# Performance work log

Hardware: AMD Instinct MI355X
Metric: run time of the kernel (lower is better)

Reference implementation:

```python
import jax, jax.numpy as jnp
import numpy as np

EPS = 1e-5


def _segment_norm(x, seg, num_segments):
    # x: [N, D], seg: [N] sorted segment ids in [0, num_segments)
    ones = jnp.ones((x.shape[0],), x.dtype)
    cnt = jax.ops.segment_sum(ones, seg, num_segments=num_segments)      # [B]
    safe = jnp.maximum(cnt, 1.0)[:, None]                                # avoid 0-div
    mean = jax.ops.segment_sum(x, seg, num_segments=num_segments) / safe # [B, D]
    centered = x - mean[seg]
    var = jax.ops.segment_sum(centered * centered, seg, num_segments=num_segments) / safe
    std = jnp.sqrt(var)                                                  # unbiased=False
    normed = centered / (std[seg] + EPS)
    # graphs with a single element are passed through unchanged
    return jnp.where((cnt > 1.0)[seg][:, None], normed, x)


def setup_inputs() -> dict:
    key = jax.random.key(0)
    k1, k2, k3, k4 = jax.random.split(key, 4)
    N, D, B = 1_000_000, 128, 1024
    node_feat = jax.random.normal(k1, (N, D), dtype=jnp.float32)
    edge_feat = jax.random.normal(k2, (N, D), dtype=jnp.float32)
    node_seg = jnp.sort(jax.random.randint(k3, (N,), 0, B, dtype=jnp.int32))
    edge_seg = jnp.sort(jax.random.randint(k4, (N,), 0, B, dtype=jnp.int32))
    return {
        "node_feat": node_feat,
        "edge_feat": edge_feat,
        "node_gamma": jnp.ones((D,), jnp.float32),
        "node_beta": jnp.zeros((D,), jnp.float32),
        "edge_gamma": jnp.ones((D,), jnp.float32),
        "edge_beta": jnp.zeros((D,), jnp.float32),
        "node_seg": node_seg,
        "edge_seg": edge_seg,
        "num_graphs": B,
    }


def reference(node_feat, edge_feat, node_gamma, node_beta, edge_gamma, edge_beta,
              node_seg, edge_seg, num_graphs):
    node_out = _segment_norm(node_feat, node_seg, num_graphs) * node_gamma + node_beta
    edge_out = _segment_norm(edge_feat, edge_seg, num_graphs) * edge_gamma + edge_beta
    return (node_out, edge_out)
```

## Files before the change

### kernel.cpp

```cpp
#include <hip/hip_runtime.h>


static constexpr int   D4     = 32;
static constexpr int   CHUNK  = 64;
static constexpr int   NCHUNK = 4;
static constexpr int   TILE_W = CHUNK * NCHUNK;
static constexpr int   TILE_B = TILE_W * 4;
static constexpr int   DEPTH  = 4;
static constexpr float EPS    = 1e-5f;

typedef float vfloat4 __attribute__((ext_vector_type(4)));

#define WAITV(N) do { asm volatile("s_waitcnt vmcnt(" #N ")" ::: "memory"); \
                      __builtin_amdgcn_sched_barrier(0); } while (0)

__device__ __forceinline__ void waitv_dyn(int n) {
    switch (n) {
        case 0:  WAITV(0);  break;
        case 4:  WAITV(4);  break;
        case 8:  WAITV(8);  break;
        case 12: WAITV(12); break;
        case 16: WAITV(16); break;
        case 20: WAITV(20); break;
        default: WAITV(24); break;
    }
}

__device__ __forceinline__ void nt_store4(float4* p, const float4& v) {
    vfloat4 w = { v.x, v.y, v.z, v.w };
    __builtin_nontemporal_store(w, reinterpret_cast<vfloat4*>(p));
}

__device__ __forceinline__ void acc4(float4& s, float4& q, const float4& v) {
    s.x += v.x; s.y += v.y; s.z += v.z; s.w += v.w;
    q.x += v.x * v.x; q.y += v.y * v.y;
    q.z += v.z * v.z; q.w += v.w * v.w;
}

__device__ __forceinline__ float4 affine4(const float4& v, const float4& A,
                                          const float4& Bc) {
    float4 o;
    o.x = v.x * A.x + Bc.x; o.y = v.y * A.y + Bc.y;
    o.z = v.z * A.z + Bc.z; o.w = v.w * A.w + Bc.w;
    return o;
}

__global__ __launch_bounds__(256) void seg_norm_deep(
    const float4* __restrict__ xn, const float4* __restrict__ xe,
    const float*  __restrict__ gn, const float*  __restrict__ bn,
    const float*  __restrict__ ge, const float*  __restrict__ be,
    const int*    __restrict__ sn, const int*    __restrict__ se,
    float4* __restrict__ on, float4* __restrict__ oe,
    int N)
{
    __shared__ float4 stage[4][DEPTH][TILE_W];
    __shared__ float4 redS[256], redQ[256];
    __shared__ int    s_bounds[2];

    const bool is_edge = (blockIdx.y != 0);
    const float4* __restrict__ x   = is_edge ? xe : xn;
    const float*  __restrict__ gam = is_edge ? ge : gn;
    const float*  __restrict__ bet = is_edge ? be : bn;
    const int*    __restrict__ seg = is_edge ? se : sn;
    float4*       __restrict__ out = is_edge ? oe : on;

    const int b   = (int)blockIdx.x;
    const int tid = (int)threadIdx.x;

    if (tid < 2) {
        const int target = b + tid;
        int lo = 0, hi = N;
        while (lo < hi) {
            int mid = (lo + hi) >> 1;
            if (seg[mid] < target) lo = mid + 1; else hi = mid;
        }
        s_bounds[tid] = lo;
    }
    __syncthreads();
    const int start = s_bounds[0];
    const int end   = s_bounds[1];
    const int cnt   = end - start;
    if (cnt <= 0) return;

    const int w    = tid >> 6;
    const int lane = tid & 63;
    const int dg   = tid & 31;

    const size_t f4base = (size_t)start * D4;
    const int    f4cnt  = cnt * D4;
    const int    nt     = f4cnt / TILE_B;

    auto issue = [&](int t, float4* lp) {
        const float4* gp = x + f4base + (size_t)t * TILE_B + w * TILE_W + lane;
        #pragma unroll
        for (int i = 0; i < NCHUNK; ++i)
            __builtin_amdgcn_global_load_lds(gp + i * CHUNK, lp + i * CHUNK, 16, 0, 0);
    };

    float4 s = make_float4(0.f, 0.f, 0.f, 0.f);
    float4 q = make_float4(0.f, 0.f, 0.f, 0.f);
    if (nt > 0) {
        const int pre = min(nt, DEPTH);
        for (int p = 0; p < pre; ++p) issue(p, &stage[w][p][0]);
        for (int t = 0; t < nt; ++t) {
            waitv_dyn(4 * min(3, nt - 1 - t));
            float4* cur = &stage[w][t & (DEPTH - 1)][0];
            #pragma unroll
            for (int i = 0; i < NCHUNK; ++i)
                acc4(s, q, cur[i * CHUNK + lane]);
            if (t + DEPTH < nt) issue(t + DEPTH, cur);
        }
    }
    for (int j = nt * TILE_B + tid; j < f4cnt; j += 256)
        acc4(s, q, x[f4base + j]);

    redS[tid] = s; redQ[tid] = q;
    __syncthreads();

    if (tid < 32) {
        float4 S = redS[tid], Q = redQ[tid];
        #pragma unroll
        for (int k = 1; k < 8; ++k) {
            const float4 a = redS[k * 32 + tid], c = redQ[k * 32 + tid];
            S.x += a.x; S.y += a.y; S.z += a.z; S.w += a.w;
            Q.x += c.x; Q.y += c.y; Q.z += c.z; Q.w += c.w;
        }
        const float rc = 1.0f / (float)cnt;
        float4 m, iv;
        m.x = S.x * rc; m.y = S.y * rc; m.z = S.z * rc; m.w = S.w * rc;
        iv.x = 1.0f / (sqrtf(fmaxf(Q.x * rc - m.x * m.x, 0.f)) + EPS);
        iv.y = 1.0f / (sqrtf(fmaxf(Q.y * rc - m.y * m.y, 0.f)) + EPS);
        iv.z = 1.0f / (sqrtf(fmaxf(Q.z * rc - m.z * m.z, 0.f)) + EPS);
        iv.w = 1.0f / (sqrtf(fmaxf(Q.w * rc - m.w * m.w, 0.f)) + EPS);
        if (cnt <= 1) {
            m = make_float4(0.f, 0.f, 0.f, 0.f);
            iv = make_float4(1.f, 1.f, 1.f, 1.f);
        }
        const float4 g4 = ((const float4*)gam)[tid];
        const float4 b4 = ((const float4*)bet)[tid];
        float4 A, Bc;
        A.x = iv.x * g4.x; A.y = iv.y * g4.y; A.z = iv.z * g4.z; A.w = iv.w * g4.w;
        Bc.x = b4.x - m.x * A.x; Bc.y = b4.y - m.y * A.y;
        Bc.z = b4.z - m.z * A.z; Bc.w = b4.w - m.w * A.w;
        redS[tid] = A; redQ[tid] = Bc;
    }
    __syncthreads();
    const float4 A  = redS[dg];
    const float4 Bc = redQ[dg];
    __syncthreads();

    if (nt > 0) {
        const int pre = min(nt, DEPTH);
        for (int p = 0; p < pre; ++p) issue(p, &stage[w][p][0]);
        for (int t = 0; t < nt; ++t) {
            waitv_dyn(4 * min(3, nt - 1 - t) + 4 * min(3, t));
            float4* cur = &stage[w][t & (DEPTH - 1)][0];
            float4* op  = out + f4base + (size_t)t * TILE_B + w * TILE_W + lane;
            #pragma unroll
            for (int i = 0; i < NCHUNK; ++i)
                nt_store4(op + i * CHUNK, affine4(cur[i * CHUNK + lane], A, Bc));
            if (t + DEPTH < nt) issue(t + DEPTH, cur);
        }
    }
    for (int j = nt * TILE_B + tid; j < f4cnt; j += 256)
        nt_store4(&out[f4base + j], affine4(x[f4base + j], A, Bc));
}

extern "C" void kernel_launch(void* const* d_in, const int* in_sizes, int n_in,
                              void* d_out, int out_size, void* d_ws, size_t ws_size,
                              hipStream_t stream) {
    const float* node_feat  = (const float*)d_in[0];
    const float* edge_feat  = (const float*)d_in[1];
    const float* node_gamma = (const float*)d_in[2];
    const float* node_beta  = (const float*)d_in[3];
    const float* edge_gamma = (const float*)d_in[4];
    const float* edge_beta  = (const float*)d_in[5];
    const int*   node_seg   = (const int*)d_in[6];
    const int*   edge_seg   = (const int*)d_in[7];

    const int D = in_sizes[2];
    const int N = in_sizes[0] / D;
    const int B = 1024;

    float* out_node = (float*)d_out;
    float* out_edge = out_node + (size_t)N * (size_t)D;

    dim3 grid((unsigned)B, 2);
    seg_norm_deep<<<grid, 256, 0, stream>>>(
        (const float4*)node_feat, (const float4*)edge_feat,
        node_gamma, node_beta, edge_gamma, edge_beta,
        node_seg, edge_seg,
        (float4*)out_node, (float4*)out_edge, N);
}
```

Baseline: 488.8 us.

## Process four segments per block, overlapping next stats pass with previous write pass

Each block now handles two node segments and two edge segments in sequence, 512 blocks instead of 2048. The statistics pass of the next segment runs in the same loop as the normalize-and-store pass of the previous one, both streaming through LDS, so reads and writes overlap within a block. This targets idle bandwidth between each segment's two phases. In exchange, grid parallelism drops to 512 blocks, per-segment pipeline depth falls from 4 to 2, and the loop has more control logic.

```diff
diff --git a/kernel.cpp b/kernel.cpp
--- a/kernel.cpp
+++ b/kernel.cpp
@@ -6,7 +6,6 @@
 static constexpr int   NCHUNK = 4;
 static constexpr int   TILE_W = CHUNK * NCHUNK;
 static constexpr int   TILE_B = TILE_W * 4;
-static constexpr int   DEPTH  = 4;
 static constexpr float EPS    = 1e-5f;
 
 typedef float vfloat4 __attribute__((ext_vector_type(4)));
@@ -45,7 +44,7 @@
     return o;
 }
 
-__global__ __launch_bounds__(256) void seg_norm_deep(
+__global__ __launch_bounds__(256) void seg_norm_k4(
     const float4* __restrict__ xn, const float4* __restrict__ xe,
     const float*  __restrict__ gn, const float*  __restrict__ bn,
     const float*  __restrict__ ge, const float*  __restrict__ be,
@@ -53,117 +52,161 @@
     float4* __restrict__ on, float4* __restrict__ oe,
     int N)
 {
-    __shared__ float4 stage[4][DEPTH][TILE_W];
+    __shared__ float4 stage[4][4][TILE_W];
     __shared__ float4 redS[256], redQ[256];
-    __shared__ int    s_bounds[2];
-
-    const bool is_edge = (blockIdx.y != 0);
-    const float4* __restrict__ x   = is_edge ? xe : xn;
-    const float*  __restrict__ gam = is_edge ? ge : gn;
-    const float*  __restrict__ bet = is_edge ? be : bn;
-    const int*    __restrict__ seg = is_edge ? se : sn;
-    float4*       __restrict__ out = is_edge ? oe : on;
-
-    const int b   = (int)blockIdx.x;
-    const int tid = (int)threadIdx.x;
-
-    if (tid < 2) {
-        const int target = b + tid;
+    __shared__ int    sb[8];
+
+    const int k    = (int)blockIdx.x;
+    const int tid  = (int)threadIdx.x;
+    const int w    = tid >> 6;
+    const int lane = tid & 63;
+    const int dg   = tid & 31;
+
+    if (tid < 8) {
+        const int t      = tid >> 1;
+        const int* sg    = (t < 2) ? sn : se;
+        const int target = 2 * k + (t & 1) + (tid & 1);
         int lo = 0, hi = N;
         while (lo < hi) {
             int mid = (lo + hi) >> 1;
-            if (seg[mid] < target) lo = mid + 1; else hi = mid;
-        }
-        s_bounds[tid] = lo;
+            if (sg[mid] < target) lo = mid + 1; else hi = mid;
+        }
+        sb[tid] = lo;
     }
     __syncthreads();
-    const int start = s_bounds[0];
-    const int end   = s_bounds[1];
-    const int cnt   = end - start;
-    if (cnt <= 0) return;
-
-    const int w    = tid >> 6;
-    const int lane = tid & 63;
-    const int dg   = tid & 31;
-
-    const size_t f4base = (size_t)start * D4;
-    const int    f4cnt  = cnt * D4;
-    const int    nt     = f4cnt / TILE_B;
-
-    auto issue = [&](int t, float4* lp) {
-        const float4* gp = x + f4base + (size_t)t * TILE_B + w * TILE_W + lane;
+
+    auto issue = [&](const float4* src, size_t fb, int t, float4* lp) {
+        const float4* gp = src + fb + (size_t)t * TILE_B + w * TILE_W + lane;
         #pragma unroll
         for (int i = 0; i < NCHUNK; ++i)
             __builtin_amdgcn_global_load_lds(gp + i * CHUNK, lp + i * CHUNK, 16, 0, 0);
     };
 
-    float4 s = make_float4(0.f, 0.f, 0.f, 0.f);
-    float4 q = make_float4(0.f, 0.f, 0.f, 0.f);
-    if (nt > 0) {
-        const int pre = min(nt, DEPTH);
-        for (int p = 0; p < pre; ++p) issue(p, &stage[w][p][0]);
-        for (int t = 0; t < nt; ++t) {
-            waitv_dyn(4 * min(3, nt - 1 - t));
-            float4* cur = &stage[w][t & (DEPTH - 1)][0];
-            #pragma unroll
-            for (int i = 0; i < NCHUNK; ++i)
-                acc4(s, q, cur[i * CHUNK + lane]);
-            if (t + DEPTH < nt) issue(t + DEPTH, cur);
+    const float4* wx = nullptr;  float4* wo = nullptr;
+    size_t wfb = 0;  int wfc = 0, wnt = 0;
+    float4 Aw = make_float4(0,0,0,0), Bw = make_float4(0,0,0,0);
+
+    for (int ph = 0; ph <= 4; ++ph) {
+        const bool hasS = (ph < 4), hasW = (ph > 0);
+
+        const float4* sx = nullptr;
+        size_t sfb = 0;  int sfc = 0, snt = 0, scnt = 0;
+        if (hasS) {
+            sx = (ph < 2) ? xn : xe;
+            const int st = sb[2 * ph], en = sb[2 * ph + 1];
+            scnt = en - st;
+            sfb  = (size_t)st * D4;
+            sfc  = scnt * D4;
+            snt  = sfc / TILE_B;
+        }
+
+        float4 s = make_float4(0,0,0,0), q = make_float4(0,0,0,0);
+
+        if (hasS && hasW) {
+            const int tmid = min(snt, wnt);
+            if (tmid > 0) {
+                issue(sx, sfb, 0, &stage[w][0][0]);
+                issue(wx, wfb, 0, &stage[w][2][0]);
+                if (tmid > 1) {
+                    issue(sx, sfb, 1, &stage[w][1][0]);
+                    issue(wx, wfb, 1, &stage[w][3][0]);
+                }
+                for (int t = 0; t < tmid; ++t) {
+                    waitv_dyn(8 * min(1, tmid - 1 - t) + 4 * min(1, t));
+                    float4* sc = &stage[w][t & 1][0];
+                    float4* wc = &stage[w][2 + (t & 1)][0];
+                    float4* op = wo + wfb + (size_t)t * TILE_B + w * TILE_W + lane;
+                    #pragma unroll
+                    for (int i = 0; i < NCHUNK; ++i) {
+                        acc4(s, q, sc[i * CHUNK + lane]);
+                        nt_store4(op + i * CHUNK,
+                                  affine4(wc[i * CHUNK + lane], Aw, Bw));
+                    }
+                    if (t + 2 < tmid) {
+                        issue(sx, sfb, t + 2, sc);
+                        issue(wx, wfb, t + 2, wc);
+                    }
+                }
+                WAITV(0);
+            }
+            for (int j = tmid * TILE_B + tid; j < sfc; j += 256)
+                acc4(s, q, sx[sfb + j]);
+            for (int j = tmid * TILE_B + tid; j < wfc; j += 256)
+                nt_store4(&wo[wfb + j], affine4(wx[wfb + j], Aw, Bw));
+        } else if (hasS) {
+            if (snt > 0) {
+                const int pre = min(snt, 4);
+                for (int p = 0; p < pre; ++p) issue(sx, sfb, p, &stage[w][p][0]);
+                for (int t = 0; t < snt; ++t) {
+                    waitv_dyn(4 * min(3, snt - 1 - t));
+                    float4* cur = &stage[w][t & 3][0];
+                    #pragma unroll
+                    for (int i = 0; i < NCHUNK; ++i)
+                        acc4(s, q, cur[i * CHUNK + lane]);
+                    if (t + 4 < snt) issue(sx, sfb, t + 4, cur);
+                }
+            }
+            for (int j = snt * TILE_B + tid; j < sfc; j += 256)
+                acc4(s, q, sx[sfb + j]);
+        } else {
+            if (wnt > 0) {
+                const int pre = min(wnt, 4);
+                for (int p = 0; p < pre; ++p) issue(wx, wfb, p, &stage[w][p][0]);
+                for (int t = 0; t < wnt; ++t) {
+                    waitv_dyn(4 * min(3, wnt - 1 - t) + 4 * min(3, t));
+                    float4* cur = &stage[w][t & 3][0];
+                    float4* op  = wo + wfb + (size_t)t * TILE_B + w * TILE_W + lane;
+                    #pragma unroll
+                    for (int i = 0; i < NCHUNK; ++i)
+                        nt_store4(op + i * CHUNK,
+                                  affine4(cur[i * CHUNK + lane], Aw, Bw));
+                    if (t + 4 < wnt) issue(wx, wfb, t + 4, cur);
+                }
+            }
+            for (int j = wnt * TILE_B + tid; j < wfc; j += 256)
+                nt_store4(&wo[wfb + j], affine4(wx[wfb + j], Aw, Bw));
+        }
+
+        if (hasS) {
+            __syncthreads();
+            redS[tid] = s; redQ[tid] = q;
+            __syncthreads();
+            if (tid < 32) {
+                float4 S = redS[tid], Q = redQ[tid];
+                #pragma unroll
+                for (int j = 1; j < 8; ++j) {
+                    const float4 a = redS[j * 32 + tid], c = redQ[j * 32 + tid];
+                    S.x += a.x; S.y += a.y; S.z += a.z; S.w += a.w;
+                    Q.x += c.x; Q.y += c.y; Q.z += c.z; Q.w += c.w;
+                }
+                const float rc = 1.0f / (float)max(scnt, 1);
+                float4 m, iv;
+                m.x = S.x * rc; m.y = S.y * rc; m.z = S.z * rc; m.w = S.w * rc;
+                iv.x = 1.0f / (sqrtf(fmaxf(Q.x * rc - m.x * m.x, 0.f)) + EPS);
+                iv.y = 1.0f / (sqrtf(fmaxf(Q.y * rc - m.y * m.y, 0.f)) + EPS);
+                iv.z = 1.0f / (sqrtf(fmaxf(Q.z * rc - m.z * m.z, 0.f)) + EPS);
+                iv.w = 1.0f / (sqrtf(fmaxf(Q.w * rc - m.w * m.w, 0.f)) + EPS);
+                if (scnt <= 1) {
+                    m  = make_float4(0.f, 0.f, 0.f, 0.f);
+                    iv = make_float4(1.f, 1.f, 1.f, 1.f);
+                }
+                const float* gm = (ph < 2) ? gn : ge;
+                const float* bt = (ph < 2) ? bn : be;
+                const float4 g4 = ((const float4*)gm)[tid];
+                const float4 b4 = ((const float4*)bt)[tid];
+                float4 A, Bc;
+                A.x = iv.x * g4.x; A.y = iv.y * g4.y;
+                A.z = iv.z * g4.z; A.w = iv.w * g4.w;
+                Bc.x = b4.x - m.x * A.x; Bc.y = b4.y - m.y * A.y;
+                Bc.z = b4.z - m.z * A.z; Bc.w = b4.w - m.w * A.w;
+                redS[tid] = A; redQ[tid] = Bc;
+            }
+            __syncthreads();
+            Aw = redS[dg]; Bw = redQ[dg];
+            wx = sx; wo = (ph < 2) ? on : oe;
+            wfb = sfb; wfc = sfc; wnt = snt;
         }
     }
-    for (int j = nt * TILE_B + tid; j < f4cnt; j += 256)
-        acc4(s, q, x[f4base + j]);
-
-    redS[tid] = s; redQ[tid] = q;
-    __syncthreads();
-
-    if (tid < 32) {
-        float4 S = redS[tid], Q = redQ[tid];
-        #pragma unroll
-        for (int k = 1; k < 8; ++k) {
-            const float4 a = redS[k * 32 + tid], c = redQ[k * 32 + tid];
-            S.x += a.x; S.y += a.y; S.z += a.z; S.w += a.w;
-            Q.x += c.x; Q.y += c.y; Q.z += c.z; Q.w += c.w;
-        }
-        const float rc = 1.0f / (float)cnt;
-        float4 m, iv;
-        m.x = S.x * rc; m.y = S.y * rc; m.z = S.z * rc; m.w = S.w * rc;
-        iv.x = 1.0f / (sqrtf(fmaxf(Q.x * rc - m.x * m.x, 0.f)) + EPS);
-        iv.y = 1.0f / (sqrtf(fmaxf(Q.y * rc - m.y * m.y, 0.f)) + EPS);
-        iv.z = 1.0f / (sqrtf(fmaxf(Q.z * rc - m.z * m.z, 0.f)) + EPS);
-        iv.w = 1.0f / (sqrtf(fmaxf(Q.w * rc - m.w * m.w, 0.f)) + EPS);
-        if (cnt <= 1) {
-            m = make_float4(0.f, 0.f, 0.f, 0.f);
-            iv = make_float4(1.f, 1.f, 1.f, 1.f);
-        }
-        const float4 g4 = ((const float4*)gam)[tid];
-        const float4 b4 = ((const float4*)bet)[tid];
-        float4 A, Bc;
-        A.x = iv.x * g4.x; A.y = iv.y * g4.y; A.z = iv.z * g4.z; A.w = iv.w * g4.w;
-        Bc.x = b4.x - m.x * A.x; Bc.y = b4.y - m.y * A.y;
-        Bc.z = b4.z - m.z * A.z; Bc.w = b4.w - m.w * A.w;
-        redS[tid] = A; redQ[tid] = Bc;
-    }
-    __syncthreads();
-    const float4 A  = redS[dg];
-    const float4 Bc = redQ[dg];
-    __syncthreads();
-
-    if (nt > 0) {
-        const int pre = min(nt, DEPTH);
-        for (int p = 0; p < pre; ++p) issue(p, &stage[w][p][0]);
-        for (int t = 0; t < nt; ++t) {
-            waitv_dyn(4 * min(3, nt - 1 - t) + 4 * min(3, t));
-            float4* cur = &stage[w][t & (DEPTH - 1)][0];
-            float4* op  = out + f4base + (size_t)t * TILE_B + w * TILE_W + lane;
-            #pragma unroll
-            for (int i = 0; i < NCHUNK; ++i)
-                nt_store4(op + i * CHUNK, affine4(cur[i * CHUNK + lane], A, Bc));
-            if (t + DEPTH < nt) issue(t + DEPTH, cur);
-        }
-    }
-    for (int j = nt * TILE_B + tid; j < f4cnt; j += 256)
-        nt_store4(&out[f4base + j], affine4(x[f4base + j], A, Bc));
 }
 
 extern "C" void kernel_launch(void* const* d_in, const int* in_sizes, int n_in,
@@ -185,8 +228,7 @@
     float* out_node = (float*)d_out;
     float* out_edge = out_node + (size_t)N * (size_t)D;
 
-    dim3 grid((unsigned)B, 2);
-    seg_norm_deep<<<grid, 256, 0, stream>>>(
+    seg_norm_k4<<<dim3((unsigned)(B / 2)), 256, 0, stream>>>(
         (const float4*)node_feat, (const float4*)edge_feat,
         node_gamma, node_beta, edge_gamma, edge_beta,
         node_seg, edge_seg,
```

New measurement: 594.8 us. 21.7% more time.

## Split block into producer stats waves and consumer normalize waves across node/edge

Applied to the files above, without the earlier changes.

Each block now handles one graph id for both node and edge features. Two waves compute sum and sum-of-squares while the other two waves wait on workgroup-scope flags, then normalize and write output. This lets the stats pass over the edge segment overlap with the normalize pass over the node segment. The cost is half the waves doing each phase, spin-waiting with s_sleep, and 1024 blocks instead of 2048, which may lower occupancy and memory parallelism.

```diff
diff --git a/kernel.cpp b/kernel.cpp
--- a/kernel.cpp
+++ b/kernel.cpp
@@ -4,8 +4,7 @@
 static constexpr int   D4     = 32;
 static constexpr int   CHUNK  = 64;
 static constexpr int   NCHUNK = 4;
-static constexpr int   TILE_W = CHUNK * NCHUNK;
-static constexpr int   TILE_B = TILE_W * 4;
+static constexpr int   TILE_W = 256;
 static constexpr int   DEPTH  = 4;
 static constexpr float EPS    = 1e-5f;
 
@@ -45,7 +44,7 @@
     return o;
 }
 
-__global__ __launch_bounds__(256) void seg_norm_deep(
+__global__ __launch_bounds__(256) void seg_norm_pc(
     const float4* __restrict__ xn, const float4* __restrict__ xe,
     const float*  __restrict__ gn, const float*  __restrict__ bn,
     const float*  __restrict__ ge, const float*  __restrict__ be,
@@ -53,117 +52,149 @@
     float4* __restrict__ on, float4* __restrict__ oe,
     int N)
 {
-    __shared__ float4 stage[4][DEPTH][TILE_W];
-    __shared__ float4 redS[256], redQ[256];
-    __shared__ int    s_bounds[2];
-
-    const bool is_edge = (blockIdx.y != 0);
-    const float4* __restrict__ x   = is_edge ? xe : xn;
-    const float*  __restrict__ gam = is_edge ? ge : gn;
-    const float*  __restrict__ bet = is_edge ? be : bn;
-    const int*    __restrict__ seg = is_edge ? se : sn;
-    float4*       __restrict__ out = is_edge ? oe : on;
-
-    const int b   = (int)blockIdx.x;
-    const int tid = (int)threadIdx.x;
-
-    if (tid < 2) {
-        const int target = b + tid;
+    __shared__ float4 ring[4][DEPTH][TILE_W];
+    __shared__ float4 pS[2][2][64], pQ[2][2][64];
+    __shared__ float4 sA[2][32], sBc[2][32];
+    __shared__ int    sb[4];
+    __shared__ int    flags[4];
+
+    const int b    = (int)blockIdx.x;
+    const int tid  = (int)threadIdx.x;
+    const int w    = tid >> 6;
+    const int lane = tid & 63;
+    const int dg   = lane & 31;
+
+    if (tid < 4) {
+        const int* sg    = (tid < 2) ? sn : se;
+        const int target = b + (tid & 1);
         int lo = 0, hi = N;
         while (lo < hi) {
             int mid = (lo + hi) >> 1;
-            if (seg[mid] < target) lo = mid + 1; else hi = mid;
+            if (sg[mid] < target) lo = mid + 1; else hi = mid;
         }
-        s_bounds[tid] = lo;
+        sb[tid] = lo;
+        flags[tid] = 0;
     }
     __syncthreads();
-    const int start = s_bounds[0];
-    const int end   = s_bounds[1];
-    const int cnt   = end - start;
-    if (cnt <= 0) return;
-
-    const int w    = tid >> 6;
-    const int lane = tid & 63;
-    const int dg   = tid & 31;
-
-    const size_t f4base = (size_t)start * D4;
-    const int    f4cnt  = cnt * D4;
-    const int    nt     = f4cnt / TILE_B;
-
-    auto issue = [&](int t, float4* lp) {
-        const float4* gp = x + f4base + (size_t)t * TILE_B + w * TILE_W + lane;
+
+    auto issue = [&](const float4* src, size_t fb, int t, float4* lp) {
+        const float4* gp = src + fb + (size_t)t * TILE_W + lane;
         #pragma unroll
         for (int i = 0; i < NCHUNK; ++i)
             __builtin_amdgcn_global_load_lds(gp + i * CHUNK, lp + i * CHUNK, 16, 0, 0);
     };
 
-    float4 s = make_float4(0.f, 0.f, 0.f, 0.f);
-    float4 q = make_float4(0.f, 0.f, 0.f, 0.f);
-    if (nt > 0) {
-        const int pre = min(nt, DEPTH);
-        for (int p = 0; p < pre; ++p) issue(p, &stage[w][p][0]);
-        for (int t = 0; t < nt; ++t) {
-            waitv_dyn(4 * min(3, nt - 1 - t));
-            float4* cur = &stage[w][t & (DEPTH - 1)][0];
-            #pragma unroll
-            for (int i = 0; i < NCHUNK; ++i)
-                acc4(s, q, cur[i * CHUNK + lane]);
-            if (t + DEPTH < nt) issue(t + DEPTH, cur);
+    if (w < 2) {
+        for (int seg = 0; seg < 2; ++seg) {
+            const float4* src = seg ? xe : xn;
+            const int st = sb[seg * 2], en = sb[seg * 2 + 1];
+            const size_t fb = (size_t)st * D4;
+            const int fc = (en - st) * D4;
+            const int nt = fc / TILE_W;
+            const int myCnt = (nt + 1 - w) / 2;
+            float4 s = make_float4(0,0,0,0), q = make_float4(0,0,0,0);
+            const int pre = min(myCnt, DEPTH);
+            for (int p = 0; p < pre; ++p)
+                issue(src, fb, w + 2 * p, &ring[w][p][0]);
+            for (int j = 0; j < myCnt; ++j) {
+                waitv_dyn(4 * min(3, myCnt - 1 - j));
+                float4* cur = &ring[w][j & 3][0];
+                #pragma unroll
+                for (int i = 0; i < NCHUNK; ++i)
+                    acc4(s, q, cur[i * CHUNK + lane]);
+                if (j + DEPTH < myCnt) issue(src, fb, w + 2 * (j + DEPTH), cur);
+            }
+            if (w == 0) {
+                for (int j2 = nt * TILE_W + lane; j2 < fc; j2 += 64)
+                    acc4(s, q, src[fb + j2]);
+            }
+            pS[seg][w][lane] = s; pQ[seg][w][lane] = q;
+            __threadfence_block();
+            if (lane == 0)
+                __hip_atomic_fetch_add(&flags[seg * 2], 1,
+                                       __ATOMIC_RELEASE, __HIP_MEMORY_SCOPE_WORKGROUP);
+        }
+    } else {
+        for (int seg = 0; seg < 2; ++seg) {
+            const float4* src = seg ? xe : xn;
+            float4*       dst = seg ? oe : on;
+            const float*  gm  = seg ? ge : gn;
+            const float*  bt  = seg ? be : bn;
+            const int st = sb[seg * 2], en = sb[seg * 2 + 1];
+            const int scnt = en - st;
+            const size_t fb = (size_t)st * D4;
+            const int fc = scnt * D4;
+            const int nt = fc / TILE_W;
+
+            while (__hip_atomic_load(&flags[seg * 2], __ATOMIC_ACQUIRE,
+                                     __HIP_MEMORY_SCOPE_WORKGROUP) < 2)
+                __builtin_amdgcn_s_sleep(8);
+
+            if (w == 2) {
+                if (lane < 32) {
+                    float4 S = pS[seg][0][lane], Q = pQ[seg][0][lane];
+                    const float4 a1 = pS[seg][0][lane + 32], c1 = pQ[seg][0][lane + 32];
+                    const float4 a2 = pS[seg][1][lane],      c2 = pQ[seg][1][lane];
+                    const float4 a3 = pS[seg][1][lane + 32], c3 = pQ[seg][1][lane + 32];
+                    S.x += a1.x + a2.x + a3.x; S.y += a1.y + a2.y + a3.y;
+                    S.z += a1.z + a2.z + a3.z; S.w += a1.w + a2.w + a3.w;
+                    Q.x += c1.x + c2.x + c3.x; Q.y += c1.y + c2.y + c3.y;
+                    Q.z += c1.z + c2.z + c3.z; Q.w += c1.w + c2.w + c3.w;
+                    const float rc = 1.0f / (float)max(scnt, 1);
+                    float4 m, iv;
+                    m.x = S.x * rc; m.y = S.y * rc; m.z = S.z * rc; m.w = S.w * rc;
+                    iv.x = 1.0f / (sqrtf(fmaxf(Q.x * rc - m.x * m.x, 0.f)) + EPS);
+                    iv.y = 1.0f / (sqrtf(fmaxf(Q.y * rc - m.y * m.y, 0.f)) + EPS);
+                    iv.z = 1.0f / (sqrtf(fmaxf(Q.z * rc - m.z * m.z, 0.f)) + EPS);
+                    iv.w = 1.0f / (sqrtf(fmaxf(Q.w * rc - m.w * m.w, 0.f)) + EPS);
+                    if (scnt <= 1) {
+                        m  = make_float4(0.f, 0.f, 0.f, 0.f);
+                        iv = make_float4(1.f, 1.f, 1.f, 1.f);
+                    }
+                    const float4 g4 = ((const float4*)gm)[lane];
+                    const float4 b4 = ((const float4*)bt)[lane];
+                    float4 A, Bc;
+                    A.x = iv.x * g4.x; A.y = iv.y * g4.y;
+                    A.z = iv.z * g4.z; A.w = iv.w * g4.w;
+                    Bc.x = b4.x - m.x * A.x; Bc.y = b4.y - m.y * A.y;
+                    Bc.z = b4.z - m.z * A.z; Bc.w = b4.w - m.w * A.w;
+                    sA[seg][lane] = A; sBc[seg][lane] = Bc;
+                }
+                __threadfence_block();
+                if (lane == 0)
+                    __hip_atomic_store(&flags[seg * 2 + 1], 1,
+                                       __ATOMIC_RELEASE, __HIP_MEMORY_SCOPE_WORKGROUP);
+            } else {
+                while (__hip_atomic_load(&flags[seg * 2 + 1], __ATOMIC_ACQUIRE,
+                                         __HIP_MEMORY_SCOPE_WORKGROUP) < 1)
+                    __builtin_amdgcn_s_sleep(8);
+            }
+            const float4 A  = sA[seg][dg];
+            const float4 Bc = sBc[seg][dg];
+
+            const int wv = w - 2;
+            const int myCnt = (nt + 1 - wv) / 2;
+            const int pre = min(myCnt, DEPTH);
+            for (int p = 0; p < pre; ++p)
+                issue(src, fb, wv + 2 * p, &ring[w][p][0]);
+            for (int j = 0; j < myCnt; ++j) {
+                waitv_dyn(4 * min(3, myCnt - 1 - j) + 4 * min(3, j));
+                float4* cur = &ring[w][j & 3][0];
+                const int t = wv + 2 * j;
+                float4* op = dst + fb + (size_t)t * TILE_W + lane;
+                #pragma unroll
+                for (int i = 0; i < NCHUNK; ++i)
+                    nt_store4(op + i * CHUNK, affine4(cur[i * CHUNK + lane], A, Bc));
+                if (j + DEPTH < myCnt) issue(src, fb, wv + 2 * (j + DEPTH), cur);
+            }
+            if (w == 2) {
+                for (int j2 = nt * TILE_W + lane; j2 < fc; j2 += 64) {
+                    const float4 Av = sA[seg][j2 & 31], Bv = sBc[seg][j2 & 31];
+                    nt_store4(&dst[fb + j2], affine4(src[fb + j2], Av, Bv));
+                }
+            }
         }
     }
-    for (int j = nt * TILE_B + tid; j < f4cnt; j += 256)
-        acc4(s, q, x[f4base + j]);
-
-    redS[tid] = s; redQ[tid] = q;
-    __syncthreads();
-
-    if (tid < 32) {
-        float4 S = redS[tid], Q = redQ[tid];
-        #pragma unroll
-        for (int k = 1; k < 8; ++k) {
-            const float4 a = redS[k * 32 + tid], c = redQ[k * 32 + tid];
-            S.x += a.x; S.y += a.y; S.z += a.z; S.w += a.w;
-            Q.x += c.x; Q.y += c.y; Q.z += c.z; Q.w += c.w;
-        }
-        const float rc = 1.0f / (float)cnt;
-        float4 m, iv;
-        m.x = S.x * rc; m.y = S.y * rc; m.z = S.z * rc; m.w = S.w * rc;
-        iv.x = 1.0f / (sqrtf(fmaxf(Q.x * rc - m.x * m.x, 0.f)) + EPS);
-        iv.y = 1.0f / (sqrtf(fmaxf(Q.y * rc - m.y * m.y, 0.f)) + EPS);
-        iv.z = 1.0f / (sqrtf(fmaxf(Q.z * rc - m.z * m.z, 0.f)) + EPS);
-        iv.w = 1.0f / (sqrtf(fmaxf(Q.w * rc - m.w * m.w, 0.f)) + EPS);
-        if (cnt <= 1) {
-            m = make_float4(0.f, 0.f, 0.f, 0.f);
-            iv = make_float4(1.f, 1.f, 1.f, 1.f);
-        }
-        const float4 g4 = ((const float4*)gam)[tid];
-        const float4 b4 = ((const float4*)bet)[tid];
-        float4 A, Bc;
-        A.x = iv.x * g4.x; A.y = iv.y * g4.y; A.z = iv.z * g4.z; A.w = iv.w * g4.w;
-        Bc.x = b4.x - m.x * A.x; Bc.y = b4.y - m.y * A.y;
-        Bc.z = b4.z - m.z * A.z; Bc.w = b4.w - m.w * A.w;
-        redS[tid] = A; redQ[tid] = Bc;
-    }
-    __syncthreads();
-    const float4 A  = redS[dg];
-    const float4 Bc = redQ[dg];
-    __syncthreads();
-
-    if (nt > 0) {
-        const int pre = min(nt, DEPTH);
-        for (int p = 0; p < pre; ++p) issue(p, &stage[w][p][0]);
-        for (int t = 0; t < nt; ++t) {
-            waitv_dyn(4 * min(3, nt - 1 - t) + 4 * min(3, t));
-            float4* cur = &stage[w][t & (DEPTH - 1)][0];
-            float4* op  = out + f4base + (size_t)t * TILE_B + w * TILE_W + lane;
-            #pragma unroll
-            for (int i = 0; i < NCHUNK; ++i)
-                nt_store4(op + i * CHUNK, affine4(cur[i * CHUNK + lane], A, Bc));
-            if (t + DEPTH < nt) issue(t + DEPTH, cur);
-        }
-    }
-    for (int j = nt * TILE_B + tid; j < f4cnt; j += 256)
-        nt_store4(&out[f4base + j], affine4(x[f4base + j], A, Bc));
 }
 
 extern "C" void kernel_launch(void* const* d_in, const int* in_sizes, int n_in,
@@ -185,8 +216,7 @@
     float* out_node = (float*)d_out;
     float* out_edge = out_node + (size_t)N * (size_t)D;
 
-    dim3 grid((unsigned)B, 2);
-    seg_norm_deep<<<grid, 256, 0, stream>>>(
+    seg_norm_pc<<<dim3((unsigned)B), 256, 0, stream>>>(
         (const float4*)node_feat, (const float4*)edge_feat,
         node_gamma, node_beta, edge_gamma, edge_beta,
         node_seg, edge_seg,
```

New measurement: 594.8 us. +21.7%, slower.
